# Performance work log

Measured on AMD Instinct MI355X. Metric: run time of the kernel, lower is better.

The kernel has to match this reference:

```python
import jax, jax.numpy as jnp
import numpy as np

UNITS = 4096
IN_FEATURES = 4096
TOT_SIZE = UNITS * IN_FEATURES
FINAL_SIZE = TOT_SIZE // 4  # divisible by 4, no padding needed
CLIP_VAL = 100.0


def unpack_ternary(pw, dtype):
    # Matches unpack_ternary_iterative2: for each byte, extract 2-bit fields
    # (lsb first), subtract 1 (codes 0,1,2,3 -> -1,0,1,2), and CONCATENATE
    # the four planes: [field0 of all bytes, field1 of all bytes, ...].
    parts = [(( (pw >> jnp.uint8(2 * i)) & jnp.uint8(3)).astype(dtype) - dtype(1))
             for i in range(4)]
    return jnp.concatenate(parts, axis=-1)


def setup_inputs() -> dict:
    key = jax.random.key(0)
    k_x, k_pw = jax.random.split(key)
    x = jax.random.normal(k_x, (8192, IN_FEATURES), dtype=jnp.float32)
    # packed ternary weights: random uint8 per the module's initializer
    pw = jax.random.randint(k_pw, (FINAL_SIZE,), 0, 256, dtype=jnp.int32).astype(jnp.uint8)
    scale = jnp.ones((UNITS,), dtype=jnp.float32)   # initializer='ones'
    bias = jnp.zeros((UNITS,), dtype=jnp.float32)   # initializer='zeros'
    return {"x": x, "pw": pw, "scale": scale, "bias": bias}


def reference(x, pw, scale, bias):
    dt = x.dtype.type
    unpacked = unpack_ternary(pw, dt)                 # [4 * FINAL_SIZE]
    w = unpacked[:TOT_SIZE].reshape(UNITS, IN_FEATURES)  # [units, in]
    y = jnp.einsum('ti,ui->tu', x, w)                 # matmul with transpose_b
    y = y * scale + bias
    y = jnp.clip(y, -dt(CLIP_VAL), dt(CLIP_VAL))
    return y
```

## Files before the change

### kernel.cpp

```cpp
#include <hip/hip_runtime.h>
#include <stdint.h>

#define MDIM 8192
#define NDIM 4096
#define KDIM 4096
#define FINAL_SZ (NDIM * KDIM / 4)
#define BM 128
#define BN 128
#define BK 64

#define CVT_BLOCKS ((MDIM * KDIM / 8) / 256)
#define UNPACK_BLOCKS ((FINAL_SZ / 8) / 256)

typedef __attribute__((ext_vector_type(8))) short short8;
typedef __attribute__((ext_vector_type(16))) float floatx16;

typedef const __attribute__((address_space(1))) void global_cv;
typedef __attribute__((address_space(3))) void lds_v;

__device__ __forceinline__ unsigned short f2bf_rne(float f) {
    union { float f; uint32_t u; } a; a.f = f;
    uint32_t u = a.u;
    u += 0x7FFFu + ((u >> 16) & 1u);
    return (unsigned short)(u >> 16);
}

__device__ __forceinline__ short code2bf(unsigned int c) {
    return (short)((0x40003F800000BF80ull >> (c * 16)) & 0xFFFFull);
}

__global__ void prep_kernel(const float* __restrict__ x, const void* __restrict__ pwv,
                            unsigned short* __restrict__ xb, unsigned short* __restrict__ wb) {
    const int b = blockIdx.x;
    if (b < CVT_BLOCKS) {
        int i = b * 256 + threadIdx.x;
        const float4* xin = (const float4*)x;
        float4 v0 = xin[2 * i];
        float4 v1 = xin[2 * i + 1];
        short8 o;
        o[0] = (short)f2bf_rne(v0.x); o[1] = (short)f2bf_rne(v0.y);
        o[2] = (short)f2bf_rne(v0.z); o[3] = (short)f2bf_rne(v0.w);
        o[4] = (short)f2bf_rne(v1.x); o[5] = (short)f2bf_rne(v1.y);
        o[6] = (short)f2bf_rne(v1.z); o[7] = (short)f2bf_rne(v1.w);
        *(short8*)(xb + (size_t)i * 8) = o;
    } else {
        unsigned int probe = ((const unsigned int*)pwv)[threadIdx.x & 63];
        bool packed = (__ballot(probe > 255u) != 0ull);

        int t = (b - CVT_BLOCKS) * 256 + threadIdx.x;
        unsigned int lo, hi;
        if (packed) {
            uint2 u = ((const uint2*)pwv)[t];
            lo = u.x; hi = u.y;
        } else {
            int4 q0 = ((const int4*)pwv)[2 * t];
            int4 q1 = ((const int4*)pwv)[2 * t + 1];
            lo = (unsigned)(q0.x & 255) | ((unsigned)(q0.y & 255) << 8)
               | ((unsigned)(q0.z & 255) << 16) | ((unsigned)(q0.w & 255) << 24);
            hi = (unsigned)(q1.x & 255) | ((unsigned)(q1.y & 255) << 8)
               | ((unsigned)(q1.z & 255) << 16) | ((unsigned)(q1.w & 255) << 24);
        }
        int j  = t << 3;
        int r  = j >> 12;
        int ci = j & 4095;
#pragma unroll
        for (int p = 0; p < 4; ++p) {
            short8 o;
            o[0] = code2bf((lo >> (2 * p)) & 3u);
            o[1] = code2bf((lo >> (8 + 2 * p)) & 3u);
            o[2] = code2bf((lo >> (16 + 2 * p)) & 3u);
            o[3] = code2bf((lo >> (24 + 2 * p)) & 3u);
            o[4] = code2bf((hi >> (2 * p)) & 3u);
            o[5] = code2bf((hi >> (8 + 2 * p)) & 3u);
            o[6] = code2bf((hi >> (16 + 2 * p)) & 3u);
            o[7] = code2bf((hi >> (24 + 2 * p)) & 3u);
            *(short8*)(wb + (((size_t)((p << 10) + r)) << 12) + ci) = o;
        }
    }
}

__global__ __launch_bounds__(256) void gemm_ternary(
    const unsigned short* __restrict__ A,
    const unsigned short* __restrict__ B,
    const float* __restrict__ scale,
    const float* __restrict__ bias,
    float* __restrict__ C) {
    __shared__ __align__(16) unsigned short lA[BM * BK];
    __shared__ __align__(16) unsigned short lB[BN * BK];

    const int tid  = threadIdx.x;
    const int lane = tid & 63;
    const int wave = tid >> 6;
    const int m0 = blockIdx.y * BM;
    const int n0 = blockIdx.x * BN;
    const int wm = (wave >> 1) * 64;
    const int wn = (wave & 1) * 64;

    const char* gA[4];
    const char* gB[4];
    unsigned short* lAd[4];
    unsigned short* lBd[4];
#pragma unroll
    for (int t = 0; t < 4; ++t) {
        int row  = wave * 32 + t * 8 + (lane >> 3);
        int clog = (lane & 7) ^ (row & 7);
        gA[t] = (const char*)(A + (size_t)(m0 + row) * KDIM) + clog * 16;
        gB[t] = (const char*)(B + (size_t)(n0 + row) * KDIM) + clog * 16;
        lAd[t] = lA + (wave * 32 + t * 8) * 64;
        lBd[t] = lB + (wave * 32 + t * 8) * 64;
    }

    floatx16 acc[2][2];
#pragma unroll
    for (int i = 0; i < 2; ++i)
#pragma unroll
        for (int j = 0; j < 2; ++j)
            acc[i][j] = (floatx16)(0.f);

    for (int k0 = 0; k0 < KDIM; k0 += BK) {
#pragma unroll
        for (int t = 0; t < 4; ++t) {
            __builtin_amdgcn_global_load_lds((global_cv*)gA[t], (lds_v*)lAd[t], 16, 0, 0);
            __builtin_amdgcn_global_load_lds((global_cv*)gB[t], (lds_v*)lBd[t], 16, 0, 0);
            gA[t] += BK * 2;
            gB[t] += BK * 2;
        }
        __syncthreads();

#pragma unroll
        for (int kt = 0; kt < 4; ++kt) {
            short8 af[2], bfr[2];
#pragma unroll
            for (int i = 0; i < 2; ++i) {
                int rowA = wm + i * 32 + (lane & 31);
                int cA   = (kt * 2 + (lane >> 5)) ^ (rowA & 7);
                af[i] = *(const short8*)(lA + rowA * 64 + cA * 8);
                int rowB = wn + i * 32 + (lane & 31);
                int cB   = (kt * 2 + (lane >> 5)) ^ (rowB & 7);
                bfr[i] = *(const short8*)(lB + rowB * 64 + cB * 8);
            }
#pragma unroll
            for (int mi = 0; mi < 2; ++mi)
#pragma unroll
                for (int ni = 0; ni < 2; ++ni)
                    acc[mi][ni] = __builtin_amdgcn_mfma_f32_32x32x16_bf16(
                        af[mi], bfr[ni], acc[mi][ni], 0, 0, 0);
        }
        __syncthreads();
    }

    float sc[2], bi[2];
#pragma unroll
    for (int ni = 0; ni < 2; ++ni) {
        int n  = n0 + wn + ni * 32 + (lane & 31);
        sc[ni] = scale[n];
        bi[ni] = bias[n];
    }
#pragma unroll
    for (int mi = 0; mi < 2; ++mi) {
#pragma unroll
        for (int r = 0; r < 16; ++r) {
            int m = m0 + wm + mi * 32 + 4 * (lane >> 5) + (r & 3) + 8 * (r >> 2);
            float* Crow = C + (size_t)m * NDIM;
#pragma unroll
            for (int ni = 0; ni < 2; ++ni) {
                int n = n0 + wn + ni * 32 + (lane & 31);
                float v = acc[mi][ni][r] * sc[ni] + bi[ni];
                v = fminf(100.f, fmaxf(-100.f, v));
                Crow[n] = v;
            }
        }
    }
}

extern "C" void kernel_launch(void* const* d_in, const int* in_sizes, int n_in,
                              void* d_out, int out_size, void* d_ws, size_t ws_size,
                              hipStream_t stream) {
    const float* x  = (const float*)d_in[0];
    const void*  pw = d_in[1];
    const float* scale = (const float*)d_in[2];
    const float* bias  = (const float*)d_in[3];
    float* out = (float*)d_out;

    unsigned short* xb = (unsigned short*)d_ws;
    unsigned short* wb = xb + (size_t)MDIM * KDIM;

    prep_kernel<<<CVT_BLOCKS + UNPACK_BLOCKS, 256, 0, stream>>>(x, pw, xb, wb);

    dim3 grid(NDIM / BN, MDIM / BM);
    gemm_ternary<<<grid, 256, 0, stream>>>(xb, wb, scale, bias, out);
}
```

Baseline: 490.4 us.

## Restructure ternary GEMM into 256x256 double-buffered tiles with 16x16 MFMA ping-pong

Grows the GEMM tile to 256x256 and uses 8 waves per block. The K loop now double-buffers LDS, prefetching stage t+2 while stage t is computed, and waits with explicit vmcnt counts instead of full syncthreads. It switches to 16x16x32 bf16 MFMAs split into four quadrant phases separated by barriers and priority bumps, and remaps block IDs for L2 locality. The aim is to raise arithmetic intensity and overlap global loads with matrix math. The cost is heavy register pressure (128 accumulator floats per lane) and fragile hand-written wait counts.

```diff
diff --git a/kernel.cpp b/kernel.cpp
--- a/kernel.cpp
+++ b/kernel.cpp
@@ -5,15 +5,16 @@
 #define NDIM 4096
 #define KDIM 4096
 #define FINAL_SZ (NDIM * KDIM / 4)
-#define BM 128
-#define BN 128
+#define BM 256
+#define BN 256
 #define BK 64
+#define NT (KDIM / BK)
 
 #define CVT_BLOCKS ((MDIM * KDIM / 8) / 256)
 #define UNPACK_BLOCKS ((FINAL_SZ / 8) / 256)
 
 typedef __attribute__((ext_vector_type(8))) short short8;
-typedef __attribute__((ext_vector_type(16))) float floatx16;
+typedef __attribute__((ext_vector_type(4))) float floatx4;
 
 typedef const __attribute__((address_space(1))) void global_cv;
 typedef __attribute__((address_space(3))) void lds_v;
@@ -79,95 +80,186 @@
     }
 }
 
-__global__ __launch_bounds__(256) void gemm_ternary(
+__device__ __forceinline__ void block_bar() {
+    asm volatile("" ::: "memory");
+    __builtin_amdgcn_s_barrier();
+    asm volatile("" ::: "memory");
+}
+
+__global__ __launch_bounds__(512, 2) void gemm_ternary(
     const unsigned short* __restrict__ A,
     const unsigned short* __restrict__ B,
     const float* __restrict__ scale,
     const float* __restrict__ bias,
     float* __restrict__ C) {
-    __shared__ __align__(16) unsigned short lA[BM * BK];
-    __shared__ __align__(16) unsigned short lB[BN * BK];
+    __shared__ __align__(16) unsigned short lA[2][BM * BK];
+    __shared__ __align__(16) unsigned short lB[2][BN * BK];
 
     const int tid  = threadIdx.x;
     const int lane = tid & 63;
     const int wave = tid >> 6;
-    const int m0 = blockIdx.y * BM;
-    const int n0 = blockIdx.x * BN;
-    const int wm = (wave >> 1) * 64;
-    const int wn = (wave & 1) * 64;
+    const int wm   = wave >> 2;
+    const int wn   = wave & 3;
+    const int l15  = lane & 15;
+    const int lq   = lane >> 4;
+    const int lx   = lane & 7;
+
+    const int bid = blockIdx.x;
+    const int wg  = ((bid & 7) << 6) | (bid >> 3);
+    const int m0  = (wg >> 4) * BM;
+    const int n0  = (wg & 15) * BN;
 
     const char* gA[4];
     const char* gB[4];
-    unsigned short* lAd[4];
-    unsigned short* lBd[4];
-#pragma unroll
-    for (int t = 0; t < 4; ++t) {
-        int row  = wave * 32 + t * 8 + (lane >> 3);
-        int clog = (lane & 7) ^ (row & 7);
-        gA[t] = (const char*)(A + (size_t)(m0 + row) * KDIM) + clog * 16;
-        gB[t] = (const char*)(B + (size_t)(n0 + row) * KDIM) + clog * 16;
-        lAd[t] = lA + (wave * 32 + t * 8) * 64;
-        lBd[t] = lB + (wave * 32 + t * 8) * 64;
-    }
-
-    floatx16 acc[2][2];
-#pragma unroll
-    for (int i = 0; i < 2; ++i)
+    int lOff[4];
+#pragma unroll
+    for (int r = 0; r < 4; ++r) {
+        int rowr = r * 64 + wave * 8 + (lane >> 3);
+        int cg   = (lane & 7) ^ ((lane >> 3) & 7);
+        gA[r] = (const char*)(A + (size_t)(m0 + rowr) * KDIM + cg * 8);
+        gB[r] = (const char*)(B + (size_t)(n0 + rowr) * KDIM + cg * 8);
+        lOff[r] = (r * 64 + wave * 8) * BK;
+    }
+
+    int cOff[2];
+#pragma unroll
+    for (int ks = 0; ks < 2; ++ks)
+        cOff[ks] = ((((ks << 2) + lq) ^ lx) << 3);
+
+    floatx4 acc[8][4];
+#pragma unroll
+    for (int i = 0; i < 8; ++i)
+#pragma unroll
+        for (int j = 0; j < 4; ++j)
+            acc[i][j] = (floatx4)(0.f);
+
+#define ISSUE8(cbuf)                                                              \
+    {                                                                             \
+        _Pragma("unroll") for (int r = 0; r < 4; ++r) {                           \
+            __builtin_amdgcn_global_load_lds((global_cv*)gA[r],                   \
+                (lds_v*)(&lA[(cbuf)][0] + lOff[r]), 16, 0, 0);                    \
+            gA[r] += BK * 2;                                                      \
+        }                                                                         \
+        _Pragma("unroll") for (int r = 0; r < 4; ++r) {                           \
+            __builtin_amdgcn_global_load_lds((global_cv*)gB[r],                   \
+                (lds_v*)(&lB[(cbuf)][0] + lOff[r]), 16, 0, 0);                    \
+            gB[r] += BK * 2;                                                      \
+        }                                                                         \
+    }
+
+    ISSUE8(0)
+    ISSUE8(1)
+    asm volatile("s_waitcnt vmcnt(8)" ::: "memory");
+    __builtin_amdgcn_s_barrier();
+    asm volatile("" ::: "memory");
+
+    for (int t = 0; t < NT; ++t) {
+        const unsigned short* LA = &lA[t & 1][0];
+        const unsigned short* LB = &lB[t & 1][0];
+        short8 a0[4][2], a1[4][2], b0[2][2], b1[2][2];
+
+#pragma unroll
+        for (int i = 0; i < 4; ++i)
+#pragma unroll
+            for (int ks = 0; ks < 2; ++ks)
+                a0[i][ks] = *(const short8*)(LA + (wm * 128 + i * 16 + l15) * BK + cOff[ks]);
 #pragma unroll
         for (int j = 0; j < 2; ++j)
-            acc[i][j] = (floatx16)(0.f);
-
-    for (int k0 = 0; k0 < KDIM; k0 += BK) {
-#pragma unroll
-        for (int t = 0; t < 4; ++t) {
-            __builtin_amdgcn_global_load_lds((global_cv*)gA[t], (lds_v*)lAd[t], 16, 0, 0);
-            __builtin_amdgcn_global_load_lds((global_cv*)gB[t], (lds_v*)lBd[t], 16, 0, 0);
-            gA[t] += BK * 2;
-            gB[t] += BK * 2;
-        }
-        __syncthreads();
-
-#pragma unroll
-        for (int kt = 0; kt < 4; ++kt) {
-            short8 af[2], bfr[2];
-#pragma unroll
-            for (int i = 0; i < 2; ++i) {
-                int rowA = wm + i * 32 + (lane & 31);
-                int cA   = (kt * 2 + (lane >> 5)) ^ (rowA & 7);
-                af[i] = *(const short8*)(lA + rowA * 64 + cA * 8);
-                int rowB = wn + i * 32 + (lane & 31);
-                int cB   = (kt * 2 + (lane >> 5)) ^ (rowB & 7);
-                bfr[i] = *(const short8*)(lB + rowB * 64 + cB * 8);
-            }
-#pragma unroll
-            for (int mi = 0; mi < 2; ++mi)
-#pragma unroll
-                for (int ni = 0; ni < 2; ++ni)
-                    acc[mi][ni] = __builtin_amdgcn_mfma_f32_32x32x16_bf16(
-                        af[mi], bfr[ni], acc[mi][ni], 0, 0, 0);
-        }
-        __syncthreads();
-    }
-
-    float sc[2], bi[2];
-#pragma unroll
-    for (int ni = 0; ni < 2; ++ni) {
-        int n  = n0 + wn + ni * 32 + (lane & 31);
-        sc[ni] = scale[n];
-        bi[ni] = bias[n];
-    }
-#pragma unroll
-    for (int mi = 0; mi < 2; ++mi) {
-#pragma unroll
-        for (int r = 0; r < 16; ++r) {
-            int m = m0 + wm + mi * 32 + 4 * (lane >> 5) + (r & 3) + 8 * (r >> 2);
-            float* Crow = C + (size_t)m * NDIM;
-#pragma unroll
-            for (int ni = 0; ni < 2; ++ni) {
-                int n = n0 + wn + ni * 32 + (lane & 31);
-                float v = acc[mi][ni][r] * sc[ni] + bi[ni];
+#pragma unroll
+            for (int ks = 0; ks < 2; ++ks)
+                b0[j][ks] = *(const short8*)(LB + (wn * 64 + j * 16 + l15) * BK + cOff[ks]);
+        block_bar();
+        __builtin_amdgcn_s_setprio(1);
+#pragma unroll
+        for (int i = 0; i < 4; ++i)
+#pragma unroll
+            for (int j = 0; j < 2; ++j)
+#pragma unroll
+                for (int ks = 0; ks < 2; ++ks)
+                    acc[i][j] = __builtin_amdgcn_mfma_f32_16x16x32_bf16(
+                        a0[i][ks], b0[j][ks], acc[i][j], 0, 0, 0);
+        __builtin_amdgcn_s_setprio(0);
+        block_bar();
+
+#pragma unroll
+        for (int j = 0; j < 2; ++j)
+#pragma unroll
+            for (int ks = 0; ks < 2; ++ks)
+                b1[j][ks] = *(const short8*)(LB + (wn * 64 + 32 + j * 16 + l15) * BK + cOff[ks]);
+        block_bar();
+        __builtin_amdgcn_s_setprio(1);
+#pragma unroll
+        for (int i = 0; i < 4; ++i)
+#pragma unroll
+            for (int j = 0; j < 2; ++j)
+#pragma unroll
+                for (int ks = 0; ks < 2; ++ks)
+                    acc[i][2 + j] = __builtin_amdgcn_mfma_f32_16x16x32_bf16(
+                        a0[i][ks], b1[j][ks], acc[i][2 + j], 0, 0, 0);
+        __builtin_amdgcn_s_setprio(0);
+        block_bar();
+
+#pragma unroll
+        for (int i = 0; i < 4; ++i)
+#pragma unroll
+            for (int ks = 0; ks < 2; ++ks)
+                a1[i][ks] = *(const short8*)(LA + (wm * 128 + 64 + i * 16 + l15) * BK + cOff[ks]);
+        block_bar();
+        __builtin_amdgcn_s_setprio(1);
+#pragma unroll
+        for (int i = 0; i < 4; ++i)
+#pragma unroll
+            for (int j = 0; j < 2; ++j)
+#pragma unroll
+                for (int ks = 0; ks < 2; ++ks)
+                    acc[4 + i][2 + j] = __builtin_amdgcn_mfma_f32_16x16x32_bf16(
+                        a1[i][ks], b1[j][ks], acc[4 + i][2 + j], 0, 0, 0);
+        __builtin_amdgcn_s_setprio(0);
+        block_bar();
+
+        __builtin_amdgcn_s_setprio(1);
+#pragma unroll
+        for (int i = 0; i < 4; ++i)
+#pragma unroll
+            for (int j = 0; j < 2; ++j)
+#pragma unroll
+                for (int ks = 0; ks < 2; ++ks)
+                    acc[4 + i][j] = __builtin_amdgcn_mfma_f32_16x16x32_bf16(
+                        a1[i][ks], b0[j][ks], acc[4 + i][j], 0, 0, 0);
+        __builtin_amdgcn_s_setprio(0);
+        block_bar();
+
+        if (t + 2 < NT) {
+            ISSUE8(t & 1)
+            asm volatile("s_waitcnt vmcnt(8)" ::: "memory");
+            __builtin_amdgcn_s_barrier();
+            asm volatile("" ::: "memory");
+        } else if (t + 1 < NT) {
+            asm volatile("s_waitcnt vmcnt(0)" ::: "memory");
+            __builtin_amdgcn_s_barrier();
+            asm volatile("" ::: "memory");
+        }
+    }
+#undef ISSUE8
+
+    float sc[4], bi[4];
+#pragma unroll
+    for (int nj = 0; nj < 4; ++nj) {
+        int n  = n0 + wn * 64 + nj * 16 + l15;
+        sc[nj] = scale[n];
+        bi[nj] = bias[n];
+    }
+#pragma unroll
+    for (int mi = 0; mi < 8; ++mi) {
+#pragma unroll
+        for (int r = 0; r < 4; ++r) {
+            int m = m0 + wm * 128 + mi * 16 + lq * 4 + r;
+            float* Crow = C + (size_t)m * NDIM + n0 + wn * 64 + l15;
+#pragma unroll
+            for (int nj = 0; nj < 4; ++nj) {
+                float v = acc[mi][nj][r] * sc[nj] + bi[nj];
                 v = fminf(100.f, fmaxf(-100.f, v));
-                Crow[n] = v;
+                Crow[nj * 16] = v;
             }
         }
     }
@@ -187,6 +279,5 @@
 
     prep_kernel<<<CVT_BLOCKS + UNPACK_BLOCKS, 256, 0, stream>>>(x, pw, xb, wb);
 
-    dim3 grid(NDIM / BN, MDIM / BM);
-    gemm_ternary<<<grid, 256, 0, stream>>>(xb, wb, scale, bias, out);
-}
+    gemm_ternary<<<dim3((MDIM / BM) * (NDIM / BN)), 512, 0, stream>>>(xb, wb, scale, bias, out);
+}
```

Result: slower. 556.0 us (+13.4%).

## Rewrite GEMM as 256x256 double-buffered tile with interleaved loads and 16x16 MFMA

Applied to the files above, without the earlier changes.

The bf16 GEMM now uses 256x256 block tiles with 8 waves and LDS double buffering. Global-to-LDS loads for the next K tile are split into four chunks, each issued between quarter-tile MFMA groups and gated by explicit vmcnt waits and barriers. MFMAs switch to 16x16x32 with raised wave priority, and the block index is remapped to an XCD-aware order for L2 reuse. This targets the load-latency stalls and low data reuse of the previous single-buffered 128x128 kernel, at the cost of higher register and LDS pressure and fragile hand-placed synchronisation.

```diff
diff --git a/kernel.cpp b/kernel.cpp
--- a/kernel.cpp
+++ b/kernel.cpp
@@ -5,15 +5,16 @@
 #define NDIM 4096
 #define KDIM 4096
 #define FINAL_SZ (NDIM * KDIM / 4)
-#define BM 128
-#define BN 128
+#define BM 256
+#define BN 256
 #define BK 64
+#define NT (KDIM / BK)
 
 #define CVT_BLOCKS ((MDIM * KDIM / 8) / 256)
 #define UNPACK_BLOCKS ((FINAL_SZ / 8) / 256)
 
 typedef __attribute__((ext_vector_type(8))) short short8;
-typedef __attribute__((ext_vector_type(16))) float floatx16;
+typedef __attribute__((ext_vector_type(4))) float floatx4;
 
 typedef const __attribute__((address_space(1))) void global_cv;
 typedef __attribute__((address_space(3))) void lds_v;
@@ -79,95 +80,156 @@
     }
 }
 
-__global__ __launch_bounds__(256) void gemm_ternary(
+#define VWAIT4 asm volatile("s_waitcnt vmcnt(4)" ::: "memory")
+#define VWAIT2 asm volatile("s_waitcnt vmcnt(2)" ::: "memory")
+#define VWAIT0 asm volatile("s_waitcnt vmcnt(0)" ::: "memory")
+#define BARX() do { asm volatile("" ::: "memory"); __builtin_amdgcn_s_barrier(); asm volatile("" ::: "memory"); } while (0)
+
+__global__ __launch_bounds__(512, 2) void gemm_ternary(
     const unsigned short* __restrict__ A,
     const unsigned short* __restrict__ B,
     const float* __restrict__ scale,
     const float* __restrict__ bias,
     float* __restrict__ C) {
-    __shared__ __align__(16) unsigned short lA[BM * BK];
-    __shared__ __align__(16) unsigned short lB[BN * BK];
+    __shared__ __align__(16) unsigned short lA[2][BM * BK];
+    __shared__ __align__(16) unsigned short lB[2][BN * BK];
 
     const int tid  = threadIdx.x;
     const int lane = tid & 63;
     const int wave = tid >> 6;
-    const int m0 = blockIdx.y * BM;
-    const int n0 = blockIdx.x * BN;
-    const int wm = (wave >> 1) * 64;
-    const int wn = (wave & 1) * 64;
-
+    const int wm   = wave >> 2;
+    const int wn   = wave & 3;
+    const int l15  = lane & 15;
+    const int lq   = lane >> 4;
+    const int lx   = lane & 7;
+
+    const int bid = blockIdx.x;
+    const int wg  = ((bid & 7) << 6) | (bid >> 3);
+    const int m0  = (wg >> 4) * BM;
+    const int n0  = (wg & 15) * BN;
+
+    const int lr = lane >> 3;
+    const int cg = (lane & 7) ^ lr;
     const char* gA[4];
     const char* gB[4];
-    unsigned short* lAd[4];
-    unsigned short* lBd[4];
-#pragma unroll
-    for (int t = 0; t < 4; ++t) {
-        int row  = wave * 32 + t * 8 + (lane >> 3);
-        int clog = (lane & 7) ^ (row & 7);
-        gA[t] = (const char*)(A + (size_t)(m0 + row) * KDIM) + clog * 16;
-        gB[t] = (const char*)(B + (size_t)(n0 + row) * KDIM) + clog * 16;
-        lAd[t] = lA + (wave * 32 + t * 8) * 64;
-        lBd[t] = lB + (wave * 32 + t * 8) * 64;
-    }
-
-    floatx16 acc[2][2];
-#pragma unroll
-    for (int i = 0; i < 2; ++i)
-#pragma unroll
-        for (int j = 0; j < 2; ++j)
-            acc[i][j] = (floatx16)(0.f);
-
-    for (int k0 = 0; k0 < KDIM; k0 += BK) {
-#pragma unroll
-        for (int t = 0; t < 4; ++t) {
-            __builtin_amdgcn_global_load_lds((global_cv*)gA[t], (lds_v*)lAd[t], 16, 0, 0);
-            __builtin_amdgcn_global_load_lds((global_cv*)gB[t], (lds_v*)lBd[t], 16, 0, 0);
-            gA[t] += BK * 2;
-            gB[t] += BK * 2;
-        }
-        __syncthreads();
-
-#pragma unroll
-        for (int kt = 0; kt < 4; ++kt) {
-            short8 af[2], bfr[2];
-#pragma unroll
-            for (int i = 0; i < 2; ++i) {
-                int rowA = wm + i * 32 + (lane & 31);
-                int cA   = (kt * 2 + (lane >> 5)) ^ (rowA & 7);
-                af[i] = *(const short8*)(lA + rowA * 64 + cA * 8);
-                int rowB = wn + i * 32 + (lane & 31);
-                int cB   = (kt * 2 + (lane >> 5)) ^ (rowB & 7);
-                bfr[i] = *(const short8*)(lB + rowB * 64 + cB * 8);
-            }
-#pragma unroll
-            for (int mi = 0; mi < 2; ++mi)
-#pragma unroll
-                for (int ni = 0; ni < 2; ++ni)
-                    acc[mi][ni] = __builtin_amdgcn_mfma_f32_32x32x16_bf16(
-                        af[mi], bfr[ni], acc[mi][ni], 0, 0, 0);
-        }
-        __syncthreads();
-    }
-
-    float sc[2], bi[2];
-#pragma unroll
-    for (int ni = 0; ni < 2; ++ni) {
-        int n  = n0 + wn + ni * 32 + (lane & 31);
-        sc[ni] = scale[n];
-        bi[ni] = bias[n];
-    }
-#pragma unroll
-    for (int mi = 0; mi < 2; ++mi) {
-#pragma unroll
-        for (int r = 0; r < 16; ++r) {
-            int m = m0 + wm + mi * 32 + 4 * (lane >> 5) + (r & 3) + 8 * (r >> 2);
-            float* Crow = C + (size_t)m * NDIM;
-#pragma unroll
-            for (int ni = 0; ni < 2; ++ni) {
-                int n = n0 + wn + ni * 32 + (lane & 31);
-                float v = acc[mi][ni][r] * sc[ni] + bi[ni];
+    int offA[4], offB[4];
+#pragma unroll
+    for (int g = 0; g < 4; ++g) {
+        const int ab = ((g & 1) << 7) + ((g >> 1) << 6) + wave * 8;
+        offA[g] = ab * BK;
+        gA[g] = (const char*)(A + (size_t)(m0 + ab + lr) * KDIM + cg * 8);
+        const int bb = ((g & 1) << 7) + ((g >> 1) << 5)
+                     + ((wave >> 2) << 6) + ((wave & 3) << 3);
+        offB[g] = bb * BK;
+        gB[g] = (const char*)(B + (size_t)(n0 + bb + lr) * KDIM + cg * 8);
+    }
+
+    int cOff[2];
+#pragma unroll
+    for (int ks = 0; ks < 2; ++ks)
+        cOff[ks] = ((((ks << 2) + lq) ^ lx) << 3);
+
+    floatx4 acc[8][4];
+#pragma unroll
+    for (int i = 0; i < 8; ++i)
+#pragma unroll
+        for (int j = 0; j < 4; ++j)
+            acc[i][j] = (floatx4)(0.f);
+
+#define SGA(g, sb) do {                                                          \
+        __builtin_amdgcn_global_load_lds((global_cv*)gA[g],                      \
+            (lds_v*)(&lA[sb][0] + offA[g]), 16, 0, 0);                           \
+        gA[g] += BK * 2; } while (0)
+#define SGB(g, sb) do {                                                          \
+        __builtin_amdgcn_global_load_lds((global_cv*)gB[g],                      \
+            (lds_v*)(&lB[sb][0] + offB[g]), 16, 0, 0);                           \
+        gB[g] += BK * 2; } while (0)
+
+#define MFMA_Q(AF, BF, MI0, NJ0)                                                 \
+    __builtin_amdgcn_s_setprio(1);                                               \
+    _Pragma("unroll") for (int i = 0; i < 4; ++i)                                \
+    _Pragma("unroll") for (int j = 0; j < 2; ++j)                                \
+    _Pragma("unroll") for (int ks = 0; ks < 2; ++ks)                             \
+        acc[(MI0) + i][(NJ0) + j] = __builtin_amdgcn_mfma_f32_16x16x32_bf16(     \
+            AF[i][ks], BF[j][ks], acc[(MI0) + i][(NJ0) + j], 0, 0, 0);           \
+    __builtin_amdgcn_s_setprio(0)
+
+#define TILE_ITER(bufv, DOSTAGE, W0STMT, W1STMT, W3STMT)                         \
+  {                                                                              \
+    const unsigned short* LA = &lA[bufv][0];                                     \
+    const unsigned short* LB = &lB[bufv][0];                                     \
+    const int sb = (bufv) ^ 1; (void)sb;                                         \
+    short8 a0[4][2], a1[4][2], b0[2][2], b1[2][2];                               \
+                   \
+    _Pragma("unroll") for (int i = 0; i < 4; ++i)                                \
+    _Pragma("unroll") for (int ks = 0; ks < 2; ++ks)                             \
+        a0[i][ks] = *(const short8*)(LA + (wm * 128 + i * 16 + l15) * BK + cOff[ks]); \
+    _Pragma("unroll") for (int j = 0; j < 2; ++j)                                \
+    _Pragma("unroll") for (int ks = 0; ks < 2; ++ks)                             \
+        b0[j][ks] = *(const short8*)(LB + (wn * 64 + j * 16 + l15) * BK + cOff[ks]);  \
+    if (DOSTAGE) { SGA(0, sb); SGA(1, sb); }                                     \
+    BARX();                                                                      \
+    MFMA_Q(a0, b0, 0, 0);                                                        \
+    W0STMT;                                                                      \
+    BARX();                                                                      \
+             \
+    _Pragma("unroll") for (int j = 0; j < 2; ++j)                                \
+    _Pragma("unroll") for (int ks = 0; ks < 2; ++ks)                             \
+        b1[j][ks] = *(const short8*)(LB + (wn * 64 + 32 + j * 16 + l15) * BK + cOff[ks]); \
+    if (DOSTAGE) { SGB(0, sb); SGB(1, sb); }                                     \
+    BARX();                                                                      \
+    MFMA_Q(a0, b1, 0, 2);                                                        \
+    W1STMT;                                                                      \
+    BARX();                                                                      \
+             \
+    _Pragma("unroll") for (int i = 0; i < 4; ++i)                                \
+    _Pragma("unroll") for (int ks = 0; ks < 2; ++ks)                             \
+        a1[i][ks] = *(const short8*)(LA + (wm * 128 + 64 + i * 16 + l15) * BK + cOff[ks]); \
+    if (DOSTAGE) { SGB(2, sb); SGB(3, sb); }                                     \
+    BARX();                                                                      \
+    MFMA_Q(a1, b1, 4, 2);                                                        \
+    BARX();                                                                      \
+                 \
+    if (DOSTAGE) { SGA(2, sb); SGA(3, sb); }                                     \
+    BARX();                                                                      \
+    MFMA_Q(a1, b0, 4, 0);                                                        \
+    W3STMT;                                                                      \
+    BARX();                                                                      \
+  }
+
+    SGA(0, 0); SGA(1, 0); SGB(0, 0); SGB(1, 0);
+    SGB(2, 0); SGB(3, 0); SGA(2, 0); SGA(3, 0);
+    VWAIT4;
+    BARX();
+
+    for (int t = 0; t < NT - 1; ++t) {
+        TILE_ITER(t & 1, 1, VWAIT4, VWAIT4, VWAIT4)
+    }
+    TILE_ITER(1, 0, VWAIT2, VWAIT0, (void)0)
+
+#undef TILE_ITER
+#undef MFMA_Q
+#undef SGA
+#undef SGB
+
+    float sc[4], bi[4];
+#pragma unroll
+    for (int nj = 0; nj < 4; ++nj) {
+        int n  = n0 + wn * 64 + nj * 16 + l15;
+        sc[nj] = scale[n];
+        bi[nj] = bias[n];
+    }
+#pragma unroll
+    for (int mi = 0; mi < 8; ++mi) {
+#pragma unroll
+        for (int r = 0; r < 4; ++r) {
+            int m = m0 + wm * 128 + mi * 16 + lq * 4 + r;
+            float* Crow = C + (size_t)m * NDIM + n0 + wn * 64 + l15;
+#pragma unroll
+            for (int nj = 0; nj < 4; ++nj) {
+                float v = acc[mi][nj][r] * sc[nj] + bi[nj];
                 v = fminf(100.f, fmaxf(-100.f, v));
-                Crow[n] = v;
+                Crow[nj * 16] = v;
             }
         }
     }
@@ -187,6 +249,5 @@
 
     prep_kernel<<<CVT_BLOCKS + UNPACK_BLOCKS, 256, 0, stream>>>(x, pw, xb, wb);
 
-    dim3 grid(NDIM / BN, MDIM / BM);
-    gemm_ternary<<<grid, 256, 0, stream>>>(xb, wb, scale, bias, out);
-}
+    gemm_ternary<<<dim3((MDIM / BM) * (NDIM / BN)), 512, 0, stream>>>(xb, wb, scale, bias, out);
+}
```

Measured after the change: 484.8 us. No clear change (-1.2%).
